# Optimization experiments

Hardware: AMD Instinct MI355X
Metric: run time of the kernel (lower is better)

## Reference

```python
import jax, jax.numpy as jnp
import numpy as np

B, S, E, H = 4, 2048, 2048, 16
D = E // H  # head_dim = 128
MAX_LEN = 2048


def _make_freqs():
    # standard RoPE frequencies: theta = 10000^{-2i/D}
    inv_freq = 1.0 / (10000.0 ** (np.arange(0, D, 2, dtype=np.float32) / D))  # [D/2]
    t = np.arange(MAX_LEN, dtype=np.float32)
    ang = np.outer(t, inv_freq)  # [max_len, D/2]
    cos = ang.reshape(1, MAX_LEN, 1, D // 2)
    return jnp.asarray(np.cos(cos)), jnp.asarray(np.sin(cos))


def setup_inputs() -> dict:
    key = jax.random.key(0)
    ks = jax.random.split(key, 10)
    sc = 1.0 / np.sqrt(E)
    freqs_cos, freqs_sin = _make_freqs()
    return {
        "x": jax.random.normal(ks[0], (B, S, E), dtype=jnp.float32),
        "freqs_cos": freqs_cos,
        "freqs_sin": freqs_sin,
        "wq": jax.random.normal(ks[1], (E, E), dtype=jnp.float32) * sc,
        "bq": jax.random.normal(ks[2], (E,), dtype=jnp.float32) * 0.01,
        "wk": jax.random.normal(ks[3], (E, E), dtype=jnp.float32) * sc,
        "bk": jax.random.normal(ks[4], (E,), dtype=jnp.float32) * 0.01,
        "wv": jax.random.normal(ks[5], (E, E), dtype=jnp.float32) * sc,
        "bv": jax.random.normal(ks[6], (E,), dtype=jnp.float32) * 0.01,
        "wo": jax.random.normal(ks[7], (E, E), dtype=jnp.float32) * sc,
        "bo": jax.random.normal(ks[8], (E,), dtype=jnp.float32) * 0.01,
    }


def _rope(t, cos, sin):
    # t: [B, S, H, D]; complex multiply on interleaved (even, odd) pairs
    tr = t.reshape(*t.shape[:-1], -1, 2)  # [B,S,H,D/2,2]
    xr, xi = tr[..., 0], tr[..., 1]
    rr = xr * cos - xi * sin
    ri = xr * sin + xi * cos
    return jnp.stack([rr, ri], axis=-1).reshape(t.shape)


def reference(x, freqs_cos, freqs_sin, wq, bq, wk, bk, wv, bv, wo, bo):
    b, s, _ = x.shape
    q = (x @ wq.T + bq).reshape(b, s, H, D)
    k = (x @ wk.T + bk).reshape(b, s, H, D)
    v = (x @ wv.T + bv).reshape(b, s, H, D)
    cos, sin = freqs_cos[:, :s], freqs_sin[:, :s]
    q = _rope(q, cos, sin)
    k = _rope(k, cos, sin)
    # FAITHFUL to source: q,k,v stay [B,S,H,D], so matmul contracts over D
    # producing per-position head-head scores [B,S,H,H] (no transpose to BHSD).
    qk = jnp.einsum("bshd,bsgd->bshg", q, k) / jnp.sqrt(jnp.float32(D))
    att = jax.nn.softmax(qk, axis=-1)
    att_out = jnp.einsum("bshg,bsgd->bshd", att, v)  # [B,S,H,D]
    # torch: transpose(1,2).contiguous().view(B,S,-1) -> h-major flatten
    att_out = jnp.transpose(att_out, (0, 2, 1, 3)).reshape(b, s, -1)
    return att_out @ wo.T + bo
```

## Files before the change

### kernel.cpp

```cpp
#include <hip/hip_runtime.h>
#include <stdint.h>

typedef unsigned short u16t;
typedef __attribute__((ext_vector_type(8))) short frag8;
typedef __attribute__((ext_vector_type(4))) float facc4;

#define S_LEN 2048
#define E_DIM 2048
#define LDSH  8192

__device__ __forceinline__ u16t f2bf(float f) {
    union { float f; uint32_t u; } c; c.f = f;
    return (u16t)((c.u + 0x7fffu + ((c.u >> 16) & 1u)) >> 16);
}

__global__ __launch_bounds__(256) void cvt_kernel(const float* __restrict__ src,
                                                  u16t* __restrict__ dst, int n4) {
    int i = blockIdx.x * 256 + threadIdx.x;
    if (i >= n4) return;
    float4 v = ((const float4*)src)[i];
    ushort4 o;
    o.x = f2bf(v.x); o.y = f2bf(v.y); o.z = f2bf(v.z); o.w = f2bf(v.w);
    ((ushort4*)dst)[i] = o;
}

__device__ __forceinline__ void gldl16(const u16t* g, u16t* l) {
    __builtin_amdgcn_global_load_lds(
        (__attribute__((address_space(1))) void*)(g),
        (__attribute__((address_space(3))) void*)(l), 16, 0, 0);
}

__device__ __forceinline__ void gemm256(const u16t* __restrict__ A,
                                        const u16t* __restrict__ B,
                                        int bm0, int bn0,
                                        u16t* lds, facc4 acc[8][4]) {
    const int t     = threadIdx.x;
    const int lane  = t & 63;
    const int wid   = t >> 6;
    const int m16   = lane & 15;
    const int quad  = lane >> 4;
    const int wid_m = wid >> 2;
    const int wid_n = wid & 3;

#pragma unroll
    for (int i = 0; i < 8; ++i)
#pragma unroll
        for (int j = 0; j < 4; ++j) acc[i][j] = facc4{0.f, 0.f, 0.f, 0.f};

    const int colA = (((wid_m << 2) + quad) ^ (m16 & 7)) << 3;
    const int colB = ((((wid_n >> 1) << 2) + quad) ^ (m16 & 7)) << 3;
    const int roA  = m16 * 64 + colA;
    const int roB  = ((wid_n & 1) * 64 + m16) * 64 + colB;

    const int cp    = (lane & 7) ^ (lane >> 3);
    const int rgrp  = cp >> 2;
    const int qq    = cp & 3;
    const int line0 = wid * 8 + (lane >> 3);
    const u16t* pA[2]; const u16t* pB[2]; int dOf[2];
#pragma unroll
    for (int ld = 0; ld < 2; ++ld) {
        const int grow = rgrp * 128 + ld * 64 + line0;
        pA[ld] = A + (size_t)(bm0 + grow) * E_DIM + qq * 8;
        pB[ld] = B + (size_t)(bn0 + grow) * E_DIM + qq * 8;
        dOf[ld] = (ld * 512 + wid * 64) * 8;
    }

#pragma unroll
    for (int ld = 0; ld < 2; ++ld) gldl16(pA[ld],      lds +         dOf[ld]);
#pragma unroll
    for (int ld = 0; ld < 2; ++ld) gldl16(pB[ld],      lds + 16384 + dOf[ld]);
#pragma unroll
    for (int ld = 0; ld < 2; ++ld) gldl16(pA[ld] + 32, lds + LDSH  + dOf[ld]);
#pragma unroll
    for (int ld = 0; ld < 2; ++ld) gldl16(pB[ld] + 32, lds + 24576 + dOf[ld]);

#define MFMA16(IB)                                                            \
    __builtin_amdgcn_s_setprio(1);                                            \
    _Pragma("unroll")                                                         \
    for (int i = 0; i < 4; ++i)                                               \
        _Pragma("unroll")                                                     \
        for (int j = 0; j < 4; ++j)                                           \
            acc[i + IB][j] = __builtin_amdgcn_mfma_f32_16x16x32_bf16(         \
                av[i], bv[j], acc[i + IB][j], 0, 0, 0);                       \
    __builtin_amdgcn_s_setprio(0);

#pragma unroll 2
    for (int t0 = 0; t0 < 32; ++t0) {
        const u16t* Lc = lds + (t0 & 1) * 32768;
        u16t* Ln       = lds + ((t0 & 1) ^ 1) * 32768;
        const int kn   = (t0 < 31) ? (t0 + 1) * 64 : 0;
        frag8 av[4], bv[4];

        gldl16(pA[0] + kn, Ln + dOf[0]);
        gldl16(pA[1] + kn, Ln + dOf[1]);
        asm volatile("s_waitcnt vmcnt(6)" ::: "memory");
        __builtin_amdgcn_s_barrier();
#pragma unroll
        for (int j = 0; j < 4; ++j) bv[j] = *(const frag8*)(Lc + 16384 + roB + j * 1024);
#pragma unroll
        for (int i = 0; i < 4; ++i) av[i] = *(const frag8*)(Lc + roA + i * 1024);
        MFMA16(0)

        gldl16(pB[0] + kn, Ln + 16384 + dOf[0]);
        gldl16(pB[1] + kn, Ln + 16384 + dOf[1]);
#pragma unroll
        for (int i = 0; i < 4; ++i) av[i] = *(const frag8*)(Lc + roA + (i + 4) * 1024);
        MFMA16(4)

        gldl16(pA[0] + kn + 32, Ln + LDSH + dOf[0]);
        gldl16(pA[1] + kn + 32, Ln + LDSH + dOf[1]);
        asm volatile("s_waitcnt vmcnt(6)" ::: "memory");
        __builtin_amdgcn_s_barrier();
#pragma unroll
        for (int j = 0; j < 4; ++j) bv[j] = *(const frag8*)(Lc + 24576 + roB + j * 1024);
#pragma unroll
        for (int i = 0; i < 4; ++i) av[i] = *(const frag8*)(Lc + LDSH + roA + i * 1024);
        MFMA16(0)

        gldl16(pB[0] + kn + 32, Ln + 24576 + dOf[0]);
        gldl16(pB[1] + kn + 32, Ln + 24576 + dOf[1]);
#pragma unroll
        for (int i = 0; i < 4; ++i) av[i] = *(const frag8*)(Lc + LDSH + roA + (i + 4) * 1024);
        MFMA16(4)
    }
#undef MFMA16

    asm volatile("s_waitcnt vmcnt(0)" ::: "memory");
}

__device__ __forceinline__ void tile_swz(int& bm0, int& bn0) {
    const int orig = blockIdx.y * 8 + blockIdx.x;
    const int swz  = (orig & 7) * 32 + (orig >> 3);
    bm0 = (swz >> 3) * 256;
    bn0 = (swz & 7) * 256;
}

struct QkvArgs {
    const u16t* w[3];
    const float* bias[3];
    u16t* out[3];
};

__global__ __launch_bounds__(512, 2)
void qkv_gemm(const u16t* __restrict__ xb, QkvArgs args,
              const float* __restrict__ fcos, const float* __restrict__ fsin) {
    __shared__ u16t lds[65536];
    facc4 acc[8][4];
    int bm0, bn0; tile_swz(bm0, bn0);
    const int z = blockIdx.z;
    gemm256(xb, args.w[z], bm0, bn0, lds, acc);

    const int t     = threadIdx.x;
    const int lane  = t & 63;
    const int m16   = lane & 15;
    const int quad  = lane >> 4;
    const int wid   = t >> 6;
    const int wid_m = wid >> 2;
    const int wid_n = wid & 3;
    const bool rope = (z < 2);
    u16t* out = args.out[z];
    const float* bias = args.bias[z];

#pragma unroll
    for (int i = 0; i < 8; ++i) {
#pragma unroll
        for (int j = 0; j < 4; ++j) {
            const int n = bn0 + wid_n * 64 + j * 16 + m16;
            const float bn_ = bias[n];
#pragma unroll
            for (int r = 0; r < 4; ++r) {
                const int m = bm0 + wid_m * 128 + i * 16 + quad * 4 + r;
                float v = acc[i][j][r] + bn_;
                const float part = __shfl_xor(v, 1, 64);
                if (rope) {
                    const int s = m & (S_LEN - 1);
                    const int p = (n & 127) >> 1;
                    const float cs = fcos[s * 64 + p];
                    const float sn = fsin[s * 64 + p];
                    v = (n & 1) ? (part * sn + v * cs) : (v * cs - part * sn);
                }
                out[(size_t)m * E_DIM + n] = f2bf(v);
            }
        }
    }
}

__global__ __launch_bounds__(512, 2)
void out_gemm(const u16t* __restrict__ sh, const u16t* __restrict__ wob,
              const float* __restrict__ bo, float* __restrict__ out) {
    __shared__ u16t lds[65536];
    facc4 acc[8][4];
    int bm0, bn0; tile_swz(bm0, bn0);
    gemm256(sh, wob, bm0, bn0, lds, acc);

    const int t     = threadIdx.x;
    const int lane  = t & 63;
    const int m16   = lane & 15;
    const int quad  = lane >> 4;
    const int wid   = t >> 6;
    const int wid_m = wid >> 2;
    const int wid_n = wid & 3;

#pragma unroll
    for (int i = 0; i < 8; ++i) {
#pragma unroll
        for (int j = 0; j < 4; ++j) {
            const int n = bn0 + wid_n * 64 + j * 16 + m16;
            const float bn_ = bo[n];
#pragma unroll
            for (int r = 0; r < 4; ++r) {
                const int m = bm0 + wid_m * 128 + i * 16 + quad * 4 + r;
                out[(size_t)m * E_DIM + n] = acc[i][j][r] + bn_;
            }
        }
    }
}

__global__ __launch_bounds__(256)
void attn_kernel(const u16t* __restrict__ qb, const u16t* __restrict__ kb,
                 const u16t* __restrict__ vb, u16t* __restrict__ sh) {
    __shared__ u16t Vs[4][16 * 136];
    __shared__ u16t Pt[4][16 * 32];

    const int t    = threadIdx.x;
    const int wid  = t >> 6;
    const int lane = t & 63;
    const int m16  = lane & 15;
    const int quad = lane >> 4;
    const int tk   = blockIdx.x * 4 + wid;
    const int b    = tk >> 11;
    const int s    = tk & (S_LEN - 1);
    const size_t row = (size_t)tk * E_DIM;

    frag8 aq[4], ak[4];
    const u16t* qrow = qb + row + m16 * 128 + quad * 8;
    const u16t* krow = kb + row + m16 * 128 + quad * 8;
#pragma unroll
    for (int ks = 0; ks < 4; ++ks) {
        aq[ks] = *(const frag8*)(qrow + ks * 32);
        ak[ks] = *(const frag8*)(krow + ks * 32);
    }

    u16t* vs = Vs[wid];
#pragma unroll
    for (int c = 0; c < 4; ++c) {
        const int e  = c * 512 + lane * 8;
        const int vr = e >> 7, vc = e & 127;
        *(uint4*)(vs + vr * 136 + vc) = *(const uint4*)(vb + row + e);
    }

    facc4 sacc = facc4{0.f, 0.f, 0.f, 0.f};
#pragma unroll
    for (int ks = 0; ks < 4; ++ks)
        sacc = __builtin_amdgcn_mfma_f32_16x16x32_bf16(aq[ks], ak[ks], sacc, 0, 0, 0);

    float p[4], mx[4], sm[4];
#pragma unroll
    for (int r = 0; r < 4; ++r) { p[r] = sacc[r] * 0.08838834764831845f; mx[r] = p[r]; }
#pragma unroll
    for (int msk = 1; msk < 16; msk <<= 1)
#pragma unroll
        for (int r = 0; r < 4; ++r) mx[r] = fmaxf(mx[r], __shfl_xor(mx[r], msk, 64));
#pragma unroll
    for (int r = 0; r < 4; ++r) { p[r] = __expf(p[r] - mx[r]); sm[r] = p[r]; }
#pragma unroll
    for (int msk = 1; msk < 16; msk <<= 1)
#pragma unroll
        for (int r = 0; r < 4; ++r) sm[r] += __shfl_xor(sm[r], msk, 64);

    u16t* pt = Pt[wid];
#pragma unroll
    for (int r = 0; r < 4; ++r)
        pt[(quad * 4 + r) * 32 + m16] = f2bf(p[r] / sm[r]);
    *(uint2*)(pt + m16 * 32 + 16 + quad * 4) = uint2{0u, 0u};

    __syncthreads();

    const frag8 aP = *(const frag8*)(pt + m16 * 32 + quad * 8);

    facc4 oacc[8];
#pragma unroll
    for (int d = 0; d < 8; ++d) oacc[d] = facc4{0.f, 0.f, 0.f, 0.f};
#pragma unroll
    for (int dblk = 0; dblk < 8; ++dblk) {
        union { u16t u[8]; frag8 f; } bb;
#pragma unroll
        for (int j = 0; j < 8; ++j)
            bb.u[j] = vs[((quad * 8 + j) & 15) * 136 + dblk * 16 + m16];
        oacc[dblk] = __builtin_amdgcn_mfma_f32_16x16x32_bf16(aP, bb.f, oacc[dblk], 0, 0, 0);
    }

    const size_t base = ((size_t)b << 22) + (size_t)(s >> 4) * E_DIM
                      + (size_t)((s & 15) * 128);
#pragma unroll
    for (int dblk = 0; dblk < 8; ++dblk) {
        const int d = dblk * 16 + m16;
#pragma unroll
        for (int r = 0; r < 4; ++r) {
            const int h = quad * 4 + r;
            sh[base + ((size_t)h << 18) + d] = f2bf(oacc[dblk][r]);
        }
    }
}

extern "C" void kernel_launch(void* const* d_in, const int* in_sizes, int n_in,
                              void* d_out, int out_size, void* d_ws, size_t ws_size,
                              hipStream_t stream) {
    const float* x    = (const float*)d_in[0];
    const float* fcos = (const float*)d_in[1];
    const float* fsin = (const float*)d_in[2];
    const float* wq   = (const float*)d_in[3];
    const float* bq   = (const float*)d_in[4];
    const float* wk   = (const float*)d_in[5];
    const float* bk   = (const float*)d_in[6];
    const float* wv   = (const float*)d_in[7];
    const float* bv   = (const float*)d_in[8];
    const float* wo   = (const float*)d_in[9];
    const float* bo   = (const float*)d_in[10];
    float* out = (float*)d_out;

    char* ws = (char*)d_ws;
    u16t* xb  = (u16t*)(ws);
    u16t* qb  = (u16t*)(ws + 33554432ull);
    u16t* kb  = (u16t*)(ws + 67108864ull);
    u16t* vb  = (u16t*)(ws + 100663296ull);
    u16t* wqb = (u16t*)(ws + 134217728ull);
    u16t* wkb = (u16t*)(ws + 142606336ull);
    u16t* wvb = (u16t*)(ws + 150994944ull);
    u16t* wob = (u16t*)(ws + 159383552ull);

    cvt_kernel<<<16384, 256, 0, stream>>>(x, xb, 4194304);
    cvt_kernel<<<4096, 256, 0, stream>>>(wq, wqb, 1048576);
    cvt_kernel<<<4096, 256, 0, stream>>>(wk, wkb, 1048576);
    cvt_kernel<<<4096, 256, 0, stream>>>(wv, wvb, 1048576);
    cvt_kernel<<<4096, 256, 0, stream>>>(wo, wob, 1048576);

    QkvArgs qa;
    qa.w[0] = wqb; qa.w[1] = wkb; qa.w[2] = wvb;
    qa.bias[0] = bq; qa.bias[1] = bk; qa.bias[2] = bv;
    qa.out[0] = qb; qa.out[1] = kb; qa.out[2] = vb;
    qkv_gemm<<<dim3(8, 32, 3), 512, 0, stream>>>(xb, qa, fcos, fsin);

    attn_kernel<<<2048, 256, 0, stream>>>(qb, kb, vb, xb);

    out_gemm<<<dim3(8, 32), 512, 0, stream>>>(xb, wob, bo, out);
}
```

Before: 499.1 us.

## Restructure GEMM main loop into deeper prefetch with barrier-bracketed MFMA phases

Rewrites the 256x256 bf16 GEMM inner loop so global-to-LDS loads are issued further ahead (prefetching up to three half-K slices before consumption) across the two LDS buffers. Each MFMA group is bracketed by workgroup barriers, in a ping-pong style schedule, so waves stay in lockstep while the loads for later slices stream in. The aim is to hide global-load latency better and interleave LDS reads, loads and MFMAs more predictably. The cost is many more barriers per iteration and a more fragile LDS-slot reuse order that must avoid overwriting data still being read.

```diff
diff --git a/kernel.cpp b/kernel.cpp
--- a/kernel.cpp
+++ b/kernel.cpp
@@ -7,7 +7,6 @@
 
 #define S_LEN 2048
 #define E_DIM 2048
-#define LDSH  8192
 
 __device__ __forceinline__ u16t f2bf(float f) {
     union { float f; uint32_t u; } c; c.f = f;
@@ -33,7 +32,7 @@
 __device__ __forceinline__ void gemm256(const u16t* __restrict__ A,
                                         const u16t* __restrict__ B,
                                         int bm0, int bn0,
-                                        u16t* lds, facc4 acc[8][4]) {
+                                        u16t* L, facc4 acc[8][4]) {
     const int t     = threadIdx.x;
     const int lane  = t & 63;
     const int wid   = t >> 6;
@@ -56,76 +55,94 @@
     const int rgrp  = cp >> 2;
     const int qq    = cp & 3;
     const int line0 = wid * 8 + (lane >> 3);
-    const u16t* pA[2]; const u16t* pB[2]; int dOf[2];
+    const u16t* pA[2]; const u16t* pB[2];
+    const int dOf0 = wid * 512;
+    const int dOf1 = 4096 + wid * 512;
 #pragma unroll
     for (int ld = 0; ld < 2; ++ld) {
         const int grow = rgrp * 128 + ld * 64 + line0;
         pA[ld] = A + (size_t)(bm0 + grow) * E_DIM + qq * 8;
         pB[ld] = B + (size_t)(bn0 + grow) * E_DIM + qq * 8;
-        dOf[ld] = (ld * 512 + wid * 64) * 8;
-    }
-
-#pragma unroll
-    for (int ld = 0; ld < 2; ++ld) gldl16(pA[ld],      lds +         dOf[ld]);
-#pragma unroll
-    for (int ld = 0; ld < 2; ++ld) gldl16(pB[ld],      lds + 16384 + dOf[ld]);
-#pragma unroll
-    for (int ld = 0; ld < 2; ++ld) gldl16(pA[ld] + 32, lds + LDSH  + dOf[ld]);
-#pragma unroll
-    for (int ld = 0; ld < 2; ++ld) gldl16(pB[ld] + 32, lds + 24576 + dOf[ld]);
-
-#define MFMA16(IB)                                                            \
-    __builtin_amdgcn_s_setprio(1);                                            \
-    _Pragma("unroll")                                                         \
-    for (int i = 0; i < 4; ++i)                                               \
-        _Pragma("unroll")                                                     \
-        for (int j = 0; j < 4; ++j)                                           \
-            acc[i + IB][j] = __builtin_amdgcn_mfma_f32_16x16x32_bf16(         \
-                av[i], bv[j], acc[i + IB][j], 0, 0, 0);                       \
-    __builtin_amdgcn_s_setprio(0);
-
-#pragma unroll 2
-    for (int t0 = 0; t0 < 32; ++t0) {
-        const u16t* Lc = lds + (t0 & 1) * 32768;
-        u16t* Ln       = lds + ((t0 & 1) ^ 1) * 32768;
-        const int kn   = (t0 < 31) ? (t0 + 1) * 64 : 0;
+    }
+
+#define STG(P, K, DST) { gldl16(P[0] + (K), (DST) + dOf0); \
+                         gldl16(P[1] + (K), (DST) + dOf1); }
+#define CBAR { asm volatile("" ::: "memory"); \
+               __builtin_amdgcn_s_barrier(); \
+               asm volatile("" ::: "memory"); }
+#define RDB(BASE) { _Pragma("unroll") \
+    for (int j = 0; j < 4; ++j) bv[j] = *(const frag8*)((BASE) + roB + j * 1024); }
+#define RDA0(BASE) { _Pragma("unroll") \
+    for (int i = 0; i < 4; ++i) av[i] = *(const frag8*)((BASE) + roA + i * 1024); }
+#define RDA4(BASE) { _Pragma("unroll") \
+    for (int i = 0; i < 4; ++i) av[i] = *(const frag8*)((BASE) + roA + (i + 4) * 1024); }
+#define MFMA16(IB) { __builtin_amdgcn_s_setprio(1); \
+    _Pragma("unroll") for (int i = 0; i < 4; ++i) \
+    _Pragma("unroll") for (int j = 0; j < 4; ++j) \
+        acc[i + IB][j] = __builtin_amdgcn_mfma_f32_16x16x32_bf16( \
+            av[i], bv[j], acc[i + IB][j], 0, 0, 0); \
+    __builtin_amdgcn_s_setprio(0); }
+
+    STG(pB, 0,  L + 16384)
+    STG(pA, 0,  L + 0)
+    STG(pB, 32, L + 24576)
+    STG(pA, 32, L + 8192)
+    STG(pB, 64, L + 32768 + 16384)
+    STG(pA, 64, L + 32768)
+    STG(pB, 96, L + 32768 + 24576)
+    asm volatile("s_waitcnt vmcnt(6)" ::: "memory");
+    CBAR
+
+#pragma unroll 1
+    for (int u = 0; u < 16; ++u) {
+        const int kO1 = u * 128 + 96;
+        const int kE2 = (u < 15) ? u * 128 + 128 : 0;
+        const int kO2 = (u < 15) ? u * 128 + 192 : 0;
         frag8 av[4], bv[4];
 
-        gldl16(pA[0] + kn, Ln + dOf[0]);
-        gldl16(pA[1] + kn, Ln + dOf[1]);
+        RDB(L + 16384) RDA0(L)
+        STG(pA, kO1, L + 32768 + 8192)
+        CBAR MFMA16(0) CBAR
+
+        RDA4(L)
+        STG(pB, kE2, L + 16384)
+        CBAR MFMA16(4) CBAR
+
+        RDB(L + 24576) RDA0(L + 8192)
+        STG(pA, kE2, L)
+        CBAR MFMA16(0) CBAR
+
+        RDA4(L + 8192)
+        STG(pB, kE2 + 32, L + 24576)
         asm volatile("s_waitcnt vmcnt(6)" ::: "memory");
-        __builtin_amdgcn_s_barrier();
-#pragma unroll
-        for (int j = 0; j < 4; ++j) bv[j] = *(const frag8*)(Lc + 16384 + roB + j * 1024);
-#pragma unroll
-        for (int i = 0; i < 4; ++i) av[i] = *(const frag8*)(Lc + roA + i * 1024);
-        MFMA16(0)
-
-        gldl16(pB[0] + kn, Ln + 16384 + dOf[0]);
-        gldl16(pB[1] + kn, Ln + 16384 + dOf[1]);
-#pragma unroll
-        for (int i = 0; i < 4; ++i) av[i] = *(const frag8*)(Lc + roA + (i + 4) * 1024);
-        MFMA16(4)
-
-        gldl16(pA[0] + kn + 32, Ln + LDSH + dOf[0]);
-        gldl16(pA[1] + kn + 32, Ln + LDSH + dOf[1]);
+        CBAR MFMA16(4) CBAR
+
+        RDB(L + 32768 + 16384) RDA0(L + 32768)
+        STG(pA, kE2 + 32, L + 8192)
+        CBAR MFMA16(0) CBAR
+
+        RDA4(L + 32768)
+        STG(pB, kO2, L + 32768 + 16384)
+        CBAR MFMA16(4) CBAR
+
+        RDB(L + 32768 + 24576) RDA0(L + 32768 + 8192)
+        STG(pA, kO2, L + 32768)
+        CBAR MFMA16(0) CBAR
+
+        RDA4(L + 32768 + 8192)
+        STG(pB, kO2 + 32, L + 32768 + 24576)
         asm volatile("s_waitcnt vmcnt(6)" ::: "memory");
-        __builtin_amdgcn_s_barrier();
-#pragma unroll
-        for (int j = 0; j < 4; ++j) bv[j] = *(const frag8*)(Lc + 24576 + roB + j * 1024);
-#pragma unroll
-        for (int i = 0; i < 4; ++i) av[i] = *(const frag8*)(Lc + LDSH + roA + i * 1024);
-        MFMA16(0)
-
-        gldl16(pB[0] + kn + 32, Ln + 24576 + dOf[0]);
-        gldl16(pB[1] + kn + 32, Ln + 24576 + dOf[1]);
-#pragma unroll
-        for (int i = 0; i < 4; ++i) av[i] = *(const frag8*)(Lc + LDSH + roA + (i + 4) * 1024);
-        MFMA16(4)
-    }
+        CBAR MFMA16(4) CBAR
+    }
+
+    asm volatile("s_waitcnt vmcnt(0)" ::: "memory");
+
+#undef STG
+#undef CBAR
+#undef RDB
+#undef RDA0
+#undef RDA4
 #undef MFMA16
-
-    asm volatile("s_waitcnt vmcnt(0)" ::: "memory");
 }
 
 __device__ __forceinline__ void tile_swz(int& bm0, int& bn0) {
```

Result: no change. 492.6 us (-1.3%).
